# Kernel tuning notes

Hardware: AMD Instinct MI355X
Metric: run time of the kernel (lower is better)

Reference implementation:

```python
import jax, jax.numpy as jnp
import numpy as np
import math

DIM = 512
HEADS = 8
DHEAD = DIM // HEADS            # 64
NB_FEATURES = int(DHEAD * math.log(DHEAD))  # 266
B, N = 2, 2048
CHUNK = 128                     # chunk size for the causal scan
EPS = 1e-4


def gaussian_orthogonal_random_matrix(nb_rows, nb_cols, rng):
    # blocks of orthogonal rows (Q^T of QR of a gaussian), scaled by chi-distributed norms
    blocks = []
    n_full = nb_rows // nb_cols
    for _ in range(n_full):
        q, _ = np.linalg.qr(rng.standard_normal((nb_cols, nb_cols)))
        blocks.append(q.T)
    rem = nb_rows - n_full * nb_cols
    if rem > 0:
        q, _ = np.linalg.qr(rng.standard_normal((nb_cols, nb_cols)))
        blocks.append(q.T[:rem])
    mat = np.concatenate(blocks, axis=0)
    multiplier = np.linalg.norm(rng.standard_normal((nb_rows, nb_cols)), axis=1)
    return (multiplier[:, None] * mat).astype(np.float32)


def setup_inputs() -> dict:
    key = jax.random.key(0)
    k1, k2, k3 = jax.random.split(key, 3)
    rng = np.random.default_rng(0)
    x = jax.random.normal(k1, (B, N, DIM), dtype=jnp.float32)
    w_qkv = jax.random.normal(k2, (DIM, 3 * DIM), dtype=jnp.float32) / math.sqrt(DIM)
    w_out = jax.random.normal(k3, (DIM, DIM), dtype=jnp.float32) / math.sqrt(DIM)
    b_out = jnp.zeros((DIM,), dtype=jnp.float32)
    proj = jnp.asarray(gaussian_orthogonal_random_matrix(NB_FEATURES, DHEAD, rng))
    return {"x": x, "w_qkv": w_qkv, "w_out": w_out, "b_out": b_out, "proj": proj}


def softmax_kernel(data, proj, is_query):
    # data: [b,h,n,d], proj: [m,d]
    d = data.shape[-1]
    data_normalizer = d ** -0.25
    ratio = proj.shape[0] ** -0.5
    data_dash = jnp.einsum('bhnd,md->bhnm', data_normalizer * data, proj)
    diag_data = jnp.sum(data * data, axis=-1, keepdims=True) * 0.5 * (data_normalizer ** 2)
    if is_query:
        stab = jnp.max(data_dash, axis=-1, keepdims=True)
    else:
        stab = jnp.max(data_dash)
    return ratio * (jnp.exp(data_dash - diag_data - stab) + EPS)


def causal_linear_attention(q, k, v, chunk=CHUNK):
    # q,k: [b,h,n,m]; v: [b,h,n,d]
    # out_n = sum_m q_nm * (sum_{i<=n} k_im v_i) / (sum_{i<=n} k_im)   (per-feature normalization,
    # identical to causal_linear_attention_noncuda), computed in chunks for memory efficiency.
    b, h, n, m = q.shape
    d = v.shape[-1]
    nc = n // chunk
    qc = jnp.moveaxis(q.reshape(b, h, nc, chunk, m), 2, 0)  # [nc,b,h,C,m]
    kc = jnp.moveaxis(k.reshape(b, h, nc, chunk, m), 2, 0)
    vc = jnp.moveaxis(v.reshape(b, h, nc, chunk, d), 2, 0)

    def step(carry, inp):
        kv_state, ksum_state = carry            # [b,h,m,d], [b,h,m]
        qch, kch, vch = inp                     # [b,h,C,m], [b,h,C,m], [b,h,C,d]
        ksum = ksum_state[:, :, None, :] + jnp.cumsum(kch, axis=2)          # [b,h,C,m]
        ctx = kv_state[:, :, None, :, :] + jnp.cumsum(
            jnp.einsum('bhcm,bhcd->bhcmd', kch, vch), axis=2)               # [b,h,C,m,d]
        out = jnp.einsum('bhcm,bhcmd->bhcd', qch, ctx / ksum[..., None])
        return (ctx[:, :, -1], ksum[:, :, -1]), out

    init = (jnp.zeros((b, h, m, d), q.dtype), jnp.zeros((b, h, m), q.dtype))
    _, outs = jax.lax.scan(step, init, (qc, kc, vc))
    return jnp.moveaxis(outs, 0, 2).reshape(b, h, n, d)


def reference(x, w_qkv, w_out, b_out, proj):
    b, n, _ = x.shape
    qkv = x @ w_qkv                                   # [b,n,3*dim]
    q, k, v = jnp.split(qkv, 3, axis=-1)
    split = lambda t: t.reshape(b, n, HEADS, DHEAD).transpose(0, 2, 1, 3)  # b h n d
    q, k, v = split(q), split(k), split(v)
    qp = softmax_kernel(q, proj, is_query=True)       # [b,h,n,m]
    kp = softmax_kernel(k, proj, is_query=False)
    out = causal_linear_attention(qp, kp, v)          # [b,h,n,d]
    out = out.transpose(0, 2, 1, 3).reshape(b, n, DIM)
    return out @ w_out + b_out
```

## Files before the change

kernel.cpp:

```cpp
#include <hip/hip_runtime.h>
#include <math.h>

#define DIMX 512
#define NHEADS 8
#define DH 64
#define MF 266
#define MP 272
#define MPS 288
#define NB 2
#define NSEQ 2048
#define NROWS (NB*NSEQ)
#define NBH 16
#define CHK 64
#define NCH 32
#define EPSF 1e-4f
#define LDT 40
#define LDP 72

typedef __attribute__((ext_vector_type(8))) short short8;
typedef __attribute__((ext_vector_type(4))) float f32x4;
typedef unsigned short ushort_t;

__device__ __forceinline__ unsigned fkey(float f){
    unsigned u = __float_as_uint(f);
    return (f < 0.0f) ? ~u : (u | 0x80000000u);
}
__device__ __forceinline__ float fdec(unsigned k){
    unsigned u = (k & 0x80000000u) ? (k & 0x7fffffffu) : ~k;
    return __uint_as_float(u);
}
__device__ __forceinline__ float b2f(ushort_t u){
    return __uint_as_float(((unsigned)u) << 16);
}

__device__ __forceinline__ void bsplit(float a, ushort_t& h, ushort_t& l){
    unsigned u = __float_as_uint(a);
    unsigned r = (u + 0x7fffu + ((u >> 16) & 1u)) & 0xffff0000u;
    h = (ushort_t)(r >> 16);
    float res = a - __uint_as_float(r);
    unsigned v = __float_as_uint(res);
    unsigned r2 = v + 0x7fffu + ((v >> 16) & 1u);
    l = (ushort_t)(r2 >> 16);
}

__global__ __launch_bounds__(256) void split_kernel(
    const float* __restrict__ A, ushort_t* __restrict__ H, ushort_t* __restrict__ L, int total4)
{
    int i = blockIdx.x * 256 + threadIdx.x;
    if (i >= total4) return;
    float4 f = ((const float4*)A)[i];
    ushort_t h0,h1,h2,h3,l0,l1,l2,l3;
    bsplit(f.x,h0,l0); bsplit(f.y,h1,l1); bsplit(f.z,h2,l2); bsplit(f.w,h3,l3);
    ((ushort4*)H)[i] = make_ushort4(h0,h1,h2,h3);
    ((ushort4*)L)[i] = make_ushort4(l0,l1,l2,l3);
}

__global__ __launch_bounds__(256) void splitT_kernel(
    const float* __restrict__ W, ushort_t* __restrict__ Th, ushort_t* __restrict__ Tl,
    int K, int N)
{
    __shared__ ushort_t Sh[64][72], Sl[64][72];
    const int k0 = blockIdx.y * 64, n0 = blockIdx.x * 64;
    const int tid = threadIdx.x;
    {
        const int kk = tid >> 4, nq = (tid & 15) * 4;
        for (int p = 0; p < 4; p++) {
            int k = p*16 + kk;
            float4 f = *(const float4*)&W[(size_t)(k0 + k)*N + n0 + nq];
            ushort_t h, l;
            bsplit(f.x,h,l); Sh[nq+0][k]=h; Sl[nq+0][k]=l;
            bsplit(f.y,h,l); Sh[nq+1][k]=h; Sl[nq+1][k]=l;
            bsplit(f.z,h,l); Sh[nq+2][k]=h; Sl[nq+2][k]=l;
            bsplit(f.w,h,l); Sh[nq+3][k]=h; Sl[nq+3][k]=l;
        }
    }
    __syncthreads();
    {
        const int n = tid >> 2, ks = (tid & 3) * 16;
        for (int q = 0; q < 2; q++) {
            uint4 vh = *(const uint4*)&Sh[n][ks + q*8];
            uint4 vl = *(const uint4*)&Sl[n][ks + q*8];
            *(uint4*)&Th[(size_t)(n0 + n)*K + k0 + ks + q*8] = vh;
            *(uint4*)&Tl[(size_t)(n0 + n)*K + k0 + ks + q*8] = vl;
        }
    }
}

__global__ __launch_bounds__(256) void splitP_kernel(
    const float* __restrict__ proj, ushort_t* __restrict__ ph, ushort_t* __restrict__ pl,
    float nrm)
{
    int idx = blockIdx.x * 256 + threadIdx.x;
    if (idx >= MPS*64/4) return;
    int m = idx >> 4, kq = (idx & 15) * 4;
    ushort4 h4 = make_ushort4(0,0,0,0), l4 = make_ushort4(0,0,0,0);
    if (m < MF) {
        float4 f = *(const float4*)&proj[m*64 + kq];
        ushort_t hh[4], ll[4];
        bsplit(f.x*nrm,hh[0],ll[0]); bsplit(f.y*nrm,hh[1],ll[1]);
        bsplit(f.z*nrm,hh[2],ll[2]); bsplit(f.w*nrm,hh[3],ll[3]);
        h4 = make_ushort4(hh[0],hh[1],hh[2],hh[3]);
        l4 = make_ushort4(ll[0],ll[1],ll[2],ll[3]);
    }
    *(ushort4*)&ph[(size_t)m*64 + kq] = h4;
    *(ushort4*)&pl[(size_t)m*64 + kq] = l4;
}

__global__ __launch_bounds__(256) void gemm_bf16s(
    const ushort_t* __restrict__ Ah, const ushort_t* __restrict__ Al,
    const ushort_t* __restrict__ Bh, const ushort_t* __restrict__ Bl,
    const float* __restrict__ bias, float* __restrict__ C,
    int M, int N, int K)
{
    __shared__ ushort_t sAh[128*LDT], sAl[128*LDT], sBh[128*LDT], sBl[128*LDT];
    const int tid = threadIdx.x;
    const int m0 = blockIdx.y * 128, n0 = blockIdx.x * 128;
    const int lane = tid & 63, w = tid >> 6;
    const int wr = w >> 1, wc = w & 1;
    const int lr = lane & 15;
    const int lsu = (lane >> 4) * 8;
    const int r = tid >> 1, sg = (tid & 1) * 16;
    const size_t gA = (size_t)(m0 + r)*K + sg;
    const size_t gB = (size_t)(n0 + r)*K + sg;

    f32x4 acc[4][4];
    #pragma unroll
    for (int i=0;i<4;i++)
        #pragma unroll
        for (int j=0;j<4;j++) acc[i][j] = (f32x4){0.f,0.f,0.f,0.f};

    for (int k0 = 0; k0 < K; k0 += 32) {
        uint4 a0 = *(const uint4*)&Ah[gA + k0];
        uint4 a1 = *(const uint4*)&Ah[gA + k0 + 8];
        uint4 a2 = *(const uint4*)&Al[gA + k0];
        uint4 a3 = *(const uint4*)&Al[gA + k0 + 8];
        uint4 b0 = *(const uint4*)&Bh[gB + k0];
        uint4 b1 = *(const uint4*)&Bh[gB + k0 + 8];
        uint4 b2 = *(const uint4*)&Bl[gB + k0];
        uint4 b3 = *(const uint4*)&Bl[gB + k0 + 8];
        __syncthreads();
        *(uint4*)&sAh[r*LDT + sg]     = a0;
        *(uint4*)&sAh[r*LDT + sg + 8] = a1;
        *(uint4*)&sAl[r*LDT + sg]     = a2;
        *(uint4*)&sAl[r*LDT + sg + 8] = a3;
        *(uint4*)&sBh[r*LDT + sg]     = b0;
        *(uint4*)&sBh[r*LDT + sg + 8] = b1;
        *(uint4*)&sBl[r*LDT + sg]     = b2;
        *(uint4*)&sBl[r*LDT + sg + 8] = b3;
        __syncthreads();
        short8 afh[4], afl[4], bfh[4], bfl[4];
        #pragma unroll
        for (int f = 0; f < 4; f++) {
            int ra = (wr*64 + f*16 + lr)*LDT + lsu;
            int rb = (wc*64 + f*16 + lr)*LDT + lsu;
            afh[f] = *(const short8*)&sAh[ra];
            afl[f] = *(const short8*)&sAl[ra];
            bfh[f] = *(const short8*)&sBh[rb];
            bfl[f] = *(const short8*)&sBl[rb];
        }
        #pragma unroll
        for (int i = 0; i < 4; i++)
            #pragma unroll
            for (int j = 0; j < 4; j++) {
                acc[i][j] = __builtin_amdgcn_mfma_f32_16x16x32_bf16(afh[i], bfh[j], acc[i][j], 0, 0, 0);
                acc[i][j] = __builtin_amdgcn_mfma_f32_16x16x32_bf16(afh[i], bfl[j], acc[i][j], 0, 0, 0);
                acc[i][j] = __builtin_amdgcn_mfma_f32_16x16x32_bf16(afl[i], bfh[j], acc[i][j], 0, 0, 0);
            }
    }
    const int crow = (lane >> 4) * 4, ccol = lane & 15;
    #pragma unroll
    for (int i = 0; i < 4; i++) {
        #pragma unroll
        for (int j = 0; j < 4; j++) {
            int col = n0 + wc*64 + j*16 + ccol;
            float bb = bias ? bias[col] : 0.f;
            #pragma unroll
            for (int rr = 0; rr < 4; rr++) {
                int row = m0 + wr*64 + i*16 + crow + rr;
                C[(size_t)row*N + col] = acc[i][j][rr] + bb;
            }
        }
    }
}

template<bool IS_Q>
__global__ __launch_bounds__(256) void feat_mfma(
    const float* __restrict__ qkv,
    const ushort_t* __restrict__ pjh, const ushort_t* __restrict__ pjl,
    ushort_t* __restrict__ oh, ushort_t* __restrict__ ol,
    float* __restrict__ diag_out, unsigned* __restrict__ gmax,
    int coff, float ratio)
{
    __shared__ ushort_t sDh[64*LDP], sDl[64*LDP];
    __shared__ ushort_t sPh[32*LDP], sPl[32*LDP];
    __shared__ float dsqs[64];
    const int tid = threadIdx.x;
    const int bh = blockIdx.y, b = bh >> 3, h = bh & 7;
    const int n0 = blockIdx.x * 64;
    {
        const int r = tid >> 2, sgq = (tid & 3) * 16;
        const float* src = &qkv[(size_t)(b*NSEQ + n0 + r)*(3*DIMX) + coff + h*DH + sgq];
        float vals[16];
        float ss = 0.f;
        #pragma unroll
        for (int p = 0; p < 4; p++) {
            float4 f = *(const float4*)&src[p*4];
            vals[p*4+0]=f.x; vals[p*4+1]=f.y; vals[p*4+2]=f.z; vals[p*4+3]=f.w;
            ss = fmaf(f.x,f.x, fmaf(f.y,f.y, fmaf(f.z,f.z, fmaf(f.w,f.w, ss))));
        }
        ss += __shfl_xor(ss, 1, 64);
        ss += __shfl_xor(ss, 2, 64);
        if ((tid & 3) == 0) dsqs[r] = ss;
        #pragma unroll
        for (int p = 0; p < 16; p++) {
            ushort_t hh2, ll2;
            bsplit(vals[p], hh2, ll2);
            sDh[r*LDP + sgq + p] = hh2;
            sDl[r*LDP + sgq + p] = ll2;
        }
    }
    __syncthreads();
    const int lane = tid & 63, w = tid >> 6;
    const int fr = lane & 15, fk = (lane >> 4) * 8;
    short8 aDh[2], aDl[2];
    #pragma unroll
    for (int ks = 0; ks < 2; ks++) {
        int ra = (w*16 + fr)*LDP + ks*32 + fk;
        aDh[ks] = *(const short8*)&sDh[ra];
        aDl[ks] = *(const short8*)&sDl[ra];
    }
    f32x4 acc[18];
    #pragma unroll
    for (int t = 0; t < 18; t++) acc[t] = (f32x4){0.f,0.f,0.f,0.f};
    #pragma unroll
    for (int it = 0; it < 9; it++) {
        const int m0 = it*32;
        __syncthreads();
        {
            int r2 = tid >> 3, sg2 = (tid & 7) * 8;
            *(uint4*)&sPh[r2*LDP + sg2] = *(const uint4*)&pjh[(size_t)(m0 + r2)*64 + sg2];
            *(uint4*)&sPl[r2*LDP + sg2] = *(const uint4*)&pjl[(size_t)(m0 + r2)*64 + sg2];
        }
        __syncthreads();
        #pragma unroll
        for (int mt = 0; mt < 2; mt++) {
            short8 bh_[2], bl_[2];
            #pragma unroll
            for (int ks = 0; ks < 2; ks++) {
                int rb = (mt*16 + fr)*LDP + ks*32 + fk;
                bh_[ks] = *(const short8*)&sPh[rb];
                bl_[ks] = *(const short8*)&sPl[rb];
            }
            #pragma unroll
            for (int ks = 0; ks < 2; ks++) {
                acc[it*2+mt] = __builtin_amdgcn_mfma_f32_16x16x32_bf16(aDh[ks], bh_[ks], acc[it*2+mt], 0, 0, 0);
                acc[it*2+mt] = __builtin_amdgcn_mfma_f32_16x16x32_bf16(aDh[ks], bl_[ks], acc[it*2+mt], 0, 0, 0);
                acc[it*2+mt] = __builtin_amdgcn_mfma_f32_16x16x32_bf16(aDl[ks], bh_[ks], acc[it*2+mt], 0, 0, 0);
            }
        }
    }
    const size_t rbase = (size_t)bh*NSEQ + n0;
    const int crow = (lane >> 4) * 4, ccol = lane & 15;
    const int rw = w*16 + crow;
    float dg0[4];
    #pragma unroll
    for (int rr = 0; rr < 4; rr++) dg0[rr] = 0.0625f * dsqs[rw + rr];

    if (IS_Q) {
        #pragma unroll
        for (int rr = 0; rr < 4; rr++) {
            float mx = -1e30f;
            #pragma unroll
            for (int t = 0; t < 18; t++) {
                bool valid = (t < 16) || (t == 16 && ccol < (MF - 256));
                if (valid) mx = fmaxf(mx, acc[t][rr]);
            }
            mx = fmaxf(mx, __shfl_xor(mx, 1, 64));
            mx = fmaxf(mx, __shfl_xor(mx, 2, 64));
            mx = fmaxf(mx, __shfl_xor(mx, 4, 64));
            mx = fmaxf(mx, __shfl_xor(mx, 8, 64));
            float sub = dg0[rr] + mx;
            ushort_t* orh = &oh[(rbase + rw + rr)*MPS + ccol];
            ushort_t* orl = &ol[(rbase + rw + rr)*MPS + ccol];
            #pragma unroll
            for (int t = 0; t < 18; t++) {
                bool valid = (t < 16) || (t == 16 && ccol < (MF - 256));
                float v = valid ? ratio*(expf(acc[t][rr] - sub) + EPSF) : 0.f;
                ushort_t hh2, ll2; bsplit(v, hh2, ll2);
                orh[t*16] = hh2; orl[t*16] = ll2;
            }
        }
    } else {
        float wmax = -1e30f;
        #pragma unroll
        for (int rr = 0; rr < 4; rr++) {
            if (ccol == 0) diag_out[rbase + rw + rr] = dg0[rr];
            ushort_t* orh = &oh[(rbase + rw + rr)*MPS + ccol];
            ushort_t* orl = &ol[(rbase + rw + rr)*MPS + ccol];
            #pragma unroll
            for (int t = 0; t < 18; t++) {
                float v = acc[t][rr];
                bool valid = (t < 16) || (t == 16 && ccol < (MF - 256));
                if (valid) wmax = fmaxf(wmax, v);
                ushort_t hh2, ll2; bsplit(v, hh2, ll2);
                orh[t*16] = hh2; orl[t*16] = ll2;
            }
        }
        #pragma unroll
        for (int o = 1; o < 64; o <<= 1) wmax = fmaxf(wmax, __shfl_xor(wmax, o, 64));
        if (lane == 0) atomicMax(gmax, fkey(wmax));
    }
}

__global__ __launch_bounds__(256) void kexp_kernel(
    ushort_t* __restrict__ kph, ushort_t* __restrict__ kpl,
    const float* __restrict__ diagk, const unsigned* __restrict__ gmax, float ratio)
{
    unsigned gid = blockIdx.x * 256u + threadIdx.x;
    if (gid >= (unsigned)(NBH*NSEQ*(MPS/4))) return;
    unsigned row = gid / (MPS/4);
    int mq = (int)(gid % (MPS/4)) * 4;
    const float stab = fdec(*gmax);
    const float dg = diagk[row];
    size_t idx = (size_t)row*MPS + mq;
    ushort4 h4 = *(const ushort4*)&kph[idx];
    ushort4 l4 = *(const ushort4*)&kpl[idx];
    float dv[4] = {b2f(h4.x)+b2f(l4.x), b2f(h4.y)+b2f(l4.y),
                   b2f(h4.z)+b2f(l4.z), b2f(h4.w)+b2f(l4.w)};
    ushort_t hh[4], ll[4];
    #pragma unroll
    for (int j = 0; j < 4; j++) {
        float kv = (mq + j < MF) ? ratio * (expf(dv[j] - dg - stab) + EPSF) : 0.f;
        bsplit(kv, hh[j], ll[j]);
    }
    *(ushort4*)&kph[idx] = make_ushort4(hh[0],hh[1],hh[2],hh[3]);
    *(ushort4*)&kpl[idx] = make_ushort4(ll[0],ll[1],ll[2],ll[3]);
}

__global__ __launch_bounds__(320) void chunk_sums_kernel(
    const ushort_t* __restrict__ kph, const ushort_t* __restrict__ kpl,
    const float* __restrict__ qkv,
    float* __restrict__ ckvT, float* __restrict__ cksum)
{
    __shared__ float vs[CHK][DH];
    const int tid = threadIdx.x;
    const int c = blockIdx.x, bh = blockIdx.y, b = bh >> 3, h = bh & 7;
    for (int idx = tid; idx < CHK*16; idx += 320) {
        int i = idx >> 4, q = idx & 15;
        *(float4*)&vs[i][q*4] =
            *(const float4*)&qkv[(size_t)(b*NSEQ + c*CHK + i)*(3*DIMX) + 2*DIMX + h*DH + q*4];
    }
    __syncthreads();
    if (tid >= 272) return;
    const int mg = tid % 68, dg = tid / 68;
    float acc[4][16] = {};
    float ks[4] = {0.f,0.f,0.f,0.f};
    const size_t kbase = (size_t)(bh*NSEQ + c*CHK)*MPS + mg*4;
    for (int i = 0; i < CHK; i++) {
        ushort4 kh = *(const ushort4*)&kph[kbase + (size_t)i*MPS];
        ushort4 kl = *(const ushort4*)&kpl[kbase + (size_t)i*MPS];
        float kr[4] = {b2f(kh.x)+b2f(kl.x), b2f(kh.y)+b2f(kl.y),
                       b2f(kh.z)+b2f(kl.z), b2f(kh.w)+b2f(kl.w)};
        if (dg == 0) { ks[0]+=kr[0]; ks[1]+=kr[1]; ks[2]+=kr[2]; ks[3]+=kr[3]; }
        #pragma unroll
        for (int t = 0; t < 4; t++) {
            float4 vv = *(const float4*)&vs[i][dg*16 + t*4];
            float vr[4] = {vv.x,vv.y,vv.z,vv.w};
            #pragma unroll
            for (int mi=0;mi<4;mi++){
                acc[mi][t*4+0] = fmaf(kr[mi], vr[0], acc[mi][t*4+0]);
                acc[mi][t*4+1] = fmaf(kr[mi], vr[1], acc[mi][t*4+1]);
                acc[mi][t*4+2] = fmaf(kr[mi], vr[2], acc[mi][t*4+2]);
                acc[mi][t*4+3] = fmaf(kr[mi], vr[3], acc[mi][t*4+3]);
            }
        }
    }
    const size_t tbase = (size_t)(bh*NCH + c)*64;
    #pragma unroll
    for (int dd = 0; dd < 16; dd++) {
        int d = dg*16 + dd;
        *(float4*)&ckvT[(tbase + d)*MP + mg*4] =
            make_float4(acc[0][dd], acc[1][dd], acc[2][dd], acc[3][dd]);
    }
    if (dg == 0) {
        #pragma unroll
        for (int mi=0;mi<4;mi++)
            cksum[(size_t)(bh*NCH + c)*MP + mg*4 + mi] = ks[mi];
    }
}

__global__ __launch_bounds__(256) void prefix_ckvT_kernel(
    const float* __restrict__ ckvT, ushort_t* __restrict__ cth, ushort_t* __restrict__ ctl)
{
    const int bh = blockIdx.y;
    const int dm = blockIdx.x * 256 + threadIdx.x;
    if (dm >= 64*MPS) return;
    const int d = dm / MPS, m = dm % MPS;
    if (m < MP) {
        float run = 0.f;
        #pragma unroll
        for (int c = 0; c < NCH; c++) {
            size_t row = (size_t)(bh*NCH + c)*64 + d;
            ushort_t h, l;
            bsplit(run, h, l);
            cth[row*MPS + m] = h; ctl[row*MPS + m] = l;
            run += ckvT[row*MP + m];
        }
    } else {
        #pragma unroll
        for (int c = 0; c < NCH; c++) {
            size_t row = (size_t)(bh*NCH + c)*64 + d;
            cth[row*MPS + m] = 0; ctl[row*MPS + m] = 0;
        }
    }
}

__global__ __launch_bounds__(320) void prefix_ksum_kernel(float* __restrict__ cksum)
{
    const int bh = blockIdx.x;
    const int m = threadIdx.x;
    if (m >= MP) return;
    float run = 0.f;
    #pragma unroll
    for (int c = 0; c < NCH; c++) {
        size_t idx = (size_t)(bh*NCH + c)*MP + m;
        float v = cksum[idx];
        cksum[idx] = run;
        run += v;
    }
}

__global__ __launch_bounds__(320) void qprime_kernel(
    ushort_t* __restrict__ qph, ushort_t* __restrict__ qpl,
    const ushort_t* __restrict__ kph, const ushort_t* __restrict__ kpl,
    const float* __restrict__ cksum)
{
    const int c = blockIdx.x, bh = blockIdx.y;
    const int m = threadIdx.x;
    if (m >= MPS) return;
    size_t base = (size_t)(bh*NSEQ + c*CHK)*MPS + m;
    if (m < MF) {
        float run = cksum[(size_t)(bh*NCH + c)*MP + m];
        for (int i = 0; i < CHK; i++) {
            size_t idx = base + (size_t)i*MPS;
            run += b2f(kph[idx]) + b2f(kpl[idx]);
            float q = b2f(qph[idx]) + b2f(qpl[idx]);
            q /= run;
            ushort_t h, l;
            bsplit(q, h, l);
            qph[idx] = h; qpl[idx] = l;
        }
    } else {
        for (int i = 0; i < CHK; i++) {
            size_t idx = base + (size_t)i*MPS;
            qph[idx] = 0; qpl[idx] = 0;
        }
    }
}

__global__ __launch_bounds__(256) void attn_mfma(
    const ushort_t* __restrict__ qph, const ushort_t* __restrict__ qpl,
    const ushort_t* __restrict__ kph, const ushort_t* __restrict__ kpl,
    const ushort_t* __restrict__ cth, const ushort_t* __restrict__ ctl,
    const float* __restrict__ qkv,
    ushort_t* __restrict__ aout_h, ushort_t* __restrict__ aout_l)
{
    __shared__ ushort_t tQh[64*LDT], tQl[64*LDT];
    __shared__ ushort_t tKh[64*LDT], tKl[64*LDT];
    __shared__ ushort_t tSh[64*LDT], tSl[64*LDT];
    __shared__ ushort_t VTh[64*LDP], VTl[64*LDP];
    __shared__ ushort_t Ph[64*LDP],  Pl[64*LDP];
    const int tid = threadIdx.x;
    const int c = blockIdx.x, bh = blockIdx.y, b = bh >> 3, hh = bh & 7;
    const size_t rowg = (size_t)bh*NSEQ + c*CHK;
    const size_t rowx = (size_t)b*NSEQ + c*CHK;
    const size_t sbase = (size_t)(bh*NCH + c)*64;

    {
        const int j = tid >> 2, dq = (tid & 3) * 16;
        const float* vsrc = &qkv[(rowx + j)*(3*DIMX) + 2*DIMX + hh*DH + dq];
        #pragma unroll
        for (int p = 0; p < 4; p++) {
            float4 f = *(const float4*)&vsrc[p*4];
            float vr[4] = {f.x,f.y,f.z,f.w};
            #pragma unroll
            for (int wv = 0; wv < 4; wv++) {
                ushort_t h, l;
                bsplit(vr[wv], h, l);
                VTh[(dq + p*4 + wv)*LDP + j] = h;
                VTl[(dq + p*4 + wv)*LDP + j] = l;
            }
        }
    }

    const int lane = tid & 63, w = tid >> 6;
    const int wr = w >> 1, wc = w & 1;
    const int fr = lane & 15, fk = (lane >> 4) * 8;
    const int srow = tid >> 2, sseg = (tid & 3) * 8;
    f32x4 accP[2][2], accO[2][2];
    #pragma unroll
    for (int i=0;i<2;i++)
        #pragma unroll
        for (int j=0;j<2;j++){ accP[i][j]=(f32x4){0,0,0,0}; accO[i][j]=(f32x4){0,0,0,0}; }

    for (int m0 = 0; m0 < MPS; m0 += 32) {
        uint4 gq_h = *(const uint4*)&qph[(rowg + srow)*MPS + m0 + sseg];
        uint4 gq_l = *(const uint4*)&qpl[(rowg + srow)*MPS + m0 + sseg];
        uint4 gk_h = *(const uint4*)&kph[(rowg + srow)*MPS + m0 + sseg];
        uint4 gk_l = *(const uint4*)&kpl[(rowg + srow)*MPS + m0 + sseg];
        uint4 gs_h = *(const uint4*)&cth[(sbase + srow)*MPS + m0 + sseg];
        uint4 gs_l = *(const uint4*)&ctl[(sbase + srow)*MPS + m0 + sseg];
        __syncthreads();
        *(uint4*)&tQh[srow*LDT + sseg] = gq_h;
        *(uint4*)&tQl[srow*LDT + sseg] = gq_l;
        *(uint4*)&tKh[srow*LDT + sseg] = gk_h;
        *(uint4*)&tKl[srow*LDT + sseg] = gk_l;
        *(uint4*)&tSh[srow*LDT + sseg] = gs_h;
        *(uint4*)&tSl[srow*LDT + sseg] = gs_l;
        __syncthreads();
        short8 aQh[2], aQl[2], bKh[2], bKl[2], bSh[2], bSl[2];
        #pragma unroll
        for (int f = 0; f < 2; f++) {
            int ra = (wr*32 + f*16 + fr)*LDT + fk;
            int rb = (wc*32 + f*16 + fr)*LDT + fk;
            aQh[f] = *(const short8*)&tQh[ra];
            aQl[f] = *(const short8*)&tQl[ra];
            bKh[f] = *(const short8*)&tKh[rb];
            bKl[f] = *(const short8*)&tKl[rb];
            bSh[f] = *(const short8*)&tSh[rb];
            bSl[f] = *(const short8*)&tSl[rb];
        }
        #pragma unroll
        for (int i = 0; i < 2; i++)
            #pragma unroll
            for (int j = 0; j < 2; j++) {
                accP[i][j] = __builtin_amdgcn_mfma_f32_16x16x32_bf16(aQh[i], bKh[j], accP[i][j], 0, 0, 0);
                accP[i][j] = __builtin_amdgcn_mfma_f32_16x16x32_bf16(aQh[i], bKl[j], accP[i][j], 0, 0, 0);
                accP[i][j] = __builtin_amdgcn_mfma_f32_16x16x32_bf16(aQl[i], bKh[j], accP[i][j], 0, 0, 0);
                accO[i][j] = __builtin_amdgcn_mfma_f32_16x16x32_bf16(aQh[i], bSh[j], accO[i][j], 0, 0, 0);
                accO[i][j] = __builtin_amdgcn_mfma_f32_16x16x32_bf16(aQh[i], bSl[j], accO[i][j], 0, 0, 0);
                accO[i][j] = __builtin_amdgcn_mfma_f32_16x16x32_bf16(aQl[i], bSh[j], accO[i][j], 0, 0, 0);
            }
    }

    __syncthreads();
    {
        const int crow = (lane >> 4) * 4, ccol = lane & 15;
        #pragma unroll
        for (int i = 0; i < 2; i++)
            #pragma unroll
            for (int j = 0; j < 2; j++) {
                int colg = wc*32 + j*16 + ccol;
                #pragma unroll
                for (int rr = 0; rr < 4; rr++) {
                    int rowg2 = wr*32 + i*16 + crow + rr;
                    float v = (colg <= rowg2) ? accP[i][j][rr] : 0.f;
                    ushort_t h, l;
                    bsplit(v, h, l);
                    Ph[rowg2*LDP + colg] = h;
                    Pl[rowg2*LDP + colg] = l;
                }
            }
    }
    __syncthreads();

    #pragma unroll
    for (int js = 0; js < 2; js++) {
        short8 aPh[2], aPl[2], bVh[2], bVl[2];
        #pragma unroll
        for (int f = 0; f < 2; f++) {
            int ra = (wr*32 + f*16 + fr)*LDP + js*32 + fk;
            int rb = (wc*32 + f*16 + fr)*LDP + js*32 + fk;
            aPh[f] = *(const short8*)&Ph[ra];
            aPl[f] = *(const short8*)&Pl[ra];
            bVh[f] = *(const short8*)&VTh[rb];
            bVl[f] = *(const short8*)&VTl[rb];
        }
        #pragma unroll
        for (int i = 0; i < 2; i++)
            #pragma unroll
            for (int j = 0; j < 2; j++) {
                accO[i][j] = __builtin_amdgcn_mfma_f32_16x16x32_bf16(aPh[i], bVh[j], accO[i][j], 0, 0, 0);
                accO[i][j] = __builtin_amdgcn_mfma_f32_16x16x32_bf16(aPh[i], bVl[j], accO[i][j], 0, 0, 0);
                accO[i][j] = __builtin_amdgcn_mfma_f32_16x16x32_bf16(aPl[i], bVh[j], accO[i][j], 0, 0, 0);
            }
    }

    {
        const int crow = (lane >> 4) * 4, ccol = lane & 15;
        #pragma unroll
        for (int i = 0; i < 2; i++)
            #pragma unroll
            for (int j = 0; j < 2; j++) {
                int d = wc*32 + j*16 + ccol;
                #pragma unroll
                for (int rr = 0; rr < 4; rr++) {
                    int row = wr*32 + i*16 + crow + rr;
                    size_t o = (rowx + row)*DIMX + hh*DH + d;
                    ushort_t h, l;
                    bsplit(accO[i][j][rr], h, l);
                    aout_h[o] = h; aout_l[o] = l;
                }
            }
    }
}

extern "C" void kernel_launch(void* const* d_in, const int* in_sizes, int n_in,
                              void* d_out, int out_size, void* d_ws, size_t ws_size,
                              hipStream_t stream)
{
    (void)in_sizes; (void)n_in; (void)out_size; (void)ws_size;
    const float* x     = (const float*)d_in[0];
    const float* w_qkv = (const float*)d_in[1];
    const float* w_out = (const float*)d_in[2];
    const float* b_out = (const float*)d_in[3];
    const float* proj  = (const float*)d_in[4];
    float* out = (float*)d_out;

    char* ws = (char*)d_ws;
    size_t off = 0;
    auto alloc = [&](size_t bytes) -> char* {
        char* p = ws + off;
        off += (bytes + 255) & ~(size_t)255;
        return p;
    };
    float* qkv       = (float*)alloc((size_t)NROWS*3*DIMX*sizeof(float));
    float* ckvT      = (float*)alloc((size_t)NBH*NCH*64*MP*sizeof(float));
    ushort_t* qph    = (ushort_t*)alloc((size_t)NBH*NSEQ*MPS*sizeof(ushort_t));
    ushort_t* qpl    = (ushort_t*)alloc((size_t)NBH*NSEQ*MPS*sizeof(ushort_t));
    ushort_t* kph    = (ushort_t*)alloc((size_t)NBH*NSEQ*MPS*sizeof(ushort_t));
    ushort_t* kpl    = (ushort_t*)alloc((size_t)NBH*NSEQ*MPS*sizeof(ushort_t));
    ushort_t* cth    = (ushort_t*)alloc((size_t)NBH*NCH*64*MPS*sizeof(ushort_t));
    ushort_t* ctl    = (ushort_t*)alloc((size_t)NBH*NCH*64*MPS*sizeof(ushort_t));
    float* cksum     = (float*)alloc((size_t)NBH*NCH*MP*sizeof(float));
    float* diagk     = (float*)alloc((size_t)NBH*NSEQ*sizeof(float));
    unsigned* gmax   = (unsigned*)alloc(256);
    ushort_t* xs_h   = (ushort_t*)alloc((size_t)NROWS*DIMX*sizeof(ushort_t));
    ushort_t* xs_l   = (ushort_t*)alloc((size_t)NROWS*DIMX*sizeof(ushort_t));
    ushort_t* wqt_h  = (ushort_t*)alloc((size_t)(3*DIMX)*DIMX*sizeof(ushort_t));
    ushort_t* wqt_l  = (ushort_t*)alloc((size_t)(3*DIMX)*DIMX*sizeof(ushort_t));
    ushort_t* wot_h  = (ushort_t*)alloc((size_t)DIMX*DIMX*sizeof(ushort_t));
    ushort_t* wot_l  = (ushort_t*)alloc((size_t)DIMX*DIMX*sizeof(ushort_t));
    ushort_t* pjh    = (ushort_t*)alloc((size_t)MPS*64*sizeof(ushort_t));
    ushort_t* pjl    = (ushort_t*)alloc((size_t)MPS*64*sizeof(ushort_t));
    ushort_t* aout_h = xs_h;
    ushort_t* aout_l = xs_l;

    const float nrm   = (float)pow(64.0, -0.25);
    const float ratio = (float)(1.0 / sqrt(266.0));

    hipMemsetAsync(gmax, 0, sizeof(unsigned), stream);
    split_kernel<<<dim3((NROWS*DIMX/4 + 255)/256), 256, 0, stream>>>(x, xs_h, xs_l, NROWS*DIMX/4);
    splitT_kernel<<<dim3(3*DIMX/64, DIMX/64), 256, 0, stream>>>(w_qkv, wqt_h, wqt_l, DIMX, 3*DIMX);
    splitT_kernel<<<dim3(DIMX/64, DIMX/64), 256, 0, stream>>>(w_out, wot_h, wot_l, DIMX, DIMX);
    splitP_kernel<<<dim3((MPS*64/4 + 255)/256), 256, 0, stream>>>(proj, pjh, pjl, nrm);
    gemm_bf16s<<<dim3(3*DIMX/128, NROWS/128), 256, 0, stream>>>(
        xs_h, xs_l, wqt_h, wqt_l, nullptr, qkv, NROWS, 3*DIMX, DIMX);
    feat_mfma<true ><<<dim3(32, 16), 256, 0, stream>>>(
        qkv, pjh, pjl, qph, qpl, nullptr, nullptr, 0, ratio);
    feat_mfma<false><<<dim3(32, 16), 256, 0, stream>>>(
        qkv, pjh, pjl, kph, kpl, diagk, gmax, DIMX, ratio);
    kexp_kernel<<<dim3((NBH*NSEQ*(MPS/4) + 255)/256), 256, 0, stream>>>(
        kph, kpl, diagk, gmax, ratio);
    chunk_sums_kernel<<<dim3(NCH, NBH), 320, 0, stream>>>(kph, kpl, qkv, ckvT, cksum);
    prefix_ckvT_kernel<<<dim3((64*MPS + 255)/256, NBH), 256, 0, stream>>>(ckvT, cth, ctl);
    prefix_ksum_kernel<<<dim3(NBH), 320, 0, stream>>>(cksum);
    qprime_kernel<<<dim3(NCH, NBH), 320, 0, stream>>>(qph, qpl, kph, kpl, cksum);
    attn_mfma<<<dim3(NCH, NBH), 256, 0, stream>>>(
        qph, qpl, kph, kpl, cth, ctl, qkv, aout_h, aout_l);
    gemm_bf16s<<<dim3(DIMX/128, NROWS/128), 256, 0, stream>>>(
        aout_h, aout_l, wot_h, wot_l, b_out, out, NROWS, DIMX, DIMX);
}
```

Before: 248.6 us.

## Stage feature and attention outputs through LDS for coalesced stores; double-buffer projection tiles

The feature kernel now double-buffers the projection tiles in one shared buffer. Each next tile's load is issued after the current tile's MFMAs, which drops one of the two barriers per iteration. The bf16 hi/lo feature outputs were previously written as scattered 2-byte global stores. They are now staged in LDS and written as 16-byte row-contiguous stores, with the lo halves packed into registers so the same LDS buffer can be reused. The attention kernel's output also goes through LDS for vectorized stores. This adds extra barriers, LDS traffic and register pressure from the 36-entry pack array.

```diff
diff --git a/kernel.cpp b/kernel.cpp
--- a/kernel.cpp
+++ b/kernel.cpp
@@ -16,6 +16,7 @@
 #define EPSF 1e-4f
 #define LDT 40
 #define LDP 72
+#define LDO 296
 
 typedef __attribute__((ext_vector_type(8))) short short8;
 typedef __attribute__((ext_vector_type(4))) float f32x4;
@@ -191,9 +192,12 @@
     float* __restrict__ diag_out, unsigned* __restrict__ gmax,
     int coff, float ratio)
 {
-    __shared__ ushort_t sDh[64*LDP], sDl[64*LDP];
-    __shared__ ushort_t sPh[32*LDP], sPl[32*LDP];
+    __shared__ ushort_t smem[64*LDO];
     __shared__ float dsqs[64];
+    ushort_t* sDh = smem;
+    ushort_t* sDl = smem + 64*LDP;
+    ushort_t* sP  = smem + 2*64*LDP;
+    ushort_t* outb = smem;
     const int tid = threadIdx.x;
     const int bh = blockIdx.y, b = bh >> 3, h = bh & 7;
     const int n0 = blockIdx.x * 64;
@@ -219,6 +223,11 @@
             sDl[r*LDP + sgq + p] = ll2;
         }
     }
+    {
+        const int r2 = tid >> 3, sg2 = (tid & 7) * 8;
+        *(uint4*)&sP[r2*LDP + sg2]        = *(const uint4*)&pjh[(size_t)r2*64 + sg2];
+        *(uint4*)&sP[2304 + r2*LDP + sg2] = *(const uint4*)&pjl[(size_t)r2*64 + sg2];
+    }
     __syncthreads();
     const int lane = tid & 63, w = tid >> 6;
     const int fr = lane & 15, fk = (lane >> 4) * 8;
@@ -234,22 +243,16 @@
     for (int t = 0; t < 18; t++) acc[t] = (f32x4){0.f,0.f,0.f,0.f};
     #pragma unroll
     for (int it = 0; it < 9; it++) {
-        const int m0 = it*32;
-        __syncthreads();
-        {
-            int r2 = tid >> 3, sg2 = (tid & 7) * 8;
-            *(uint4*)&sPh[r2*LDP + sg2] = *(const uint4*)&pjh[(size_t)(m0 + r2)*64 + sg2];
-            *(uint4*)&sPl[r2*LDP + sg2] = *(const uint4*)&pjl[(size_t)(m0 + r2)*64 + sg2];
-        }
-        __syncthreads();
+        const ushort_t* bufh = sP + (it & 1) * 4608;
+        const ushort_t* bufl = bufh + 2304;
         #pragma unroll
         for (int mt = 0; mt < 2; mt++) {
             short8 bh_[2], bl_[2];
             #pragma unroll
             for (int ks = 0; ks < 2; ks++) {
                 int rb = (mt*16 + fr)*LDP + ks*32 + fk;
-                bh_[ks] = *(const short8*)&sPh[rb];
-                bl_[ks] = *(const short8*)&sPl[rb];
+                bh_[ks] = *(const short8*)&bufh[rb];
+                bl_[ks] = *(const short8*)&bufl[rb];
             }
             #pragma unroll
             for (int ks = 0; ks < 2; ks++) {
@@ -258,6 +261,13 @@
                 acc[it*2+mt] = __builtin_amdgcn_mfma_f32_16x16x32_bf16(aDl[ks], bh_[ks], acc[it*2+mt], 0, 0, 0);
             }
         }
+        if (it < 8) {
+            const int r2 = tid >> 3, sg2 = (tid & 7) * 8;
+            ushort_t* nb = sP + ((it+1) & 1) * 4608;
+            *(uint4*)&nb[r2*LDP + sg2]        = *(const uint4*)&pjh[(size_t)((it+1)*32 + r2)*64 + sg2];
+            *(uint4*)&nb[2304 + r2*LDP + sg2] = *(const uint4*)&pjl[(size_t)((it+1)*32 + r2)*64 + sg2];
+        }
+        __syncthreads();
     }
     const size_t rbase = (size_t)bh*NSEQ + n0;
     const int crow = (lane >> 4) * 4, ccol = lane & 15;
@@ -265,6 +275,7 @@
     float dg0[4];
     #pragma unroll
     for (int rr = 0; rr < 4; rr++) dg0[rr] = 0.0625f * dsqs[rw + rr];
+    unsigned lpack[36];
 
     if (IS_Q) {
         #pragma unroll
@@ -280,14 +291,14 @@
             mx = fmaxf(mx, __shfl_xor(mx, 4, 64));
             mx = fmaxf(mx, __shfl_xor(mx, 8, 64));
             float sub = dg0[rr] + mx;
-            ushort_t* orh = &oh[(rbase + rw + rr)*MPS + ccol];
-            ushort_t* orl = &ol[(rbase + rw + rr)*MPS + ccol];
             #pragma unroll
             for (int t = 0; t < 18; t++) {
                 bool valid = (t < 16) || (t == 16 && ccol < (MF - 256));
                 float v = valid ? ratio*(expf(acc[t][rr] - sub) + EPSF) : 0.f;
                 ushort_t hh2, ll2; bsplit(v, hh2, ll2);
-                orh[t*16] = hh2; orl[t*16] = ll2;
+                outb[(rw + rr)*LDO + t*16 + ccol] = hh2;
+                if ((t & 1) == 0) lpack[rr*9 + t/2] = ll2;
+                else              lpack[rr*9 + t/2] |= ((unsigned)ll2) << 16;
             }
         }
     } else {
@@ -295,20 +306,41 @@
         #pragma unroll
         for (int rr = 0; rr < 4; rr++) {
             if (ccol == 0) diag_out[rbase + rw + rr] = dg0[rr];
-            ushort_t* orh = &oh[(rbase + rw + rr)*MPS + ccol];
-            ushort_t* orl = &ol[(rbase + rw + rr)*MPS + ccol];
             #pragma unroll
             for (int t = 0; t < 18; t++) {
                 float v = acc[t][rr];
                 bool valid = (t < 16) || (t == 16 && ccol < (MF - 256));
                 if (valid) wmax = fmaxf(wmax, v);
                 ushort_t hh2, ll2; bsplit(v, hh2, ll2);
-                orh[t*16] = hh2; orl[t*16] = ll2;
+                outb[(rw + rr)*LDO + t*16 + ccol] = hh2;
+                if ((t & 1) == 0) lpack[rr*9 + t/2] = ll2;
+                else              lpack[rr*9 + t/2] |= ((unsigned)ll2) << 16;
             }
         }
         #pragma unroll
         for (int o = 1; o < 64; o <<= 1) wmax = fmaxf(wmax, __shfl_xor(wmax, o, 64));
         if (lane == 0) atomicMax(gmax, fkey(wmax));
+    }
+    __syncthreads();
+    #pragma unroll
+    for (int p = 0; p < 9; p++) {
+        int u = tid + p*256;
+        int row = u / 36, c8 = u % 36;
+        *(uint4*)&oh[(rbase + row)*MPS + c8*8] = *(const uint4*)&outb[row*LDO + c8*8];
+    }
+    __syncthreads();
+    #pragma unroll
+    for (int rr = 0; rr < 4; rr++)
+        #pragma unroll
+        for (int t = 0; t < 18; t++)
+            outb[(rw + rr)*LDO + t*16 + ccol] =
+                (ushort_t)((lpack[rr*9 + t/2] >> (16*(t & 1))) & 0xffffu);
+    __syncthreads();
+    #pragma unroll
+    for (int p = 0; p < 9; p++) {
+        int u = tid + p*256;
+        int row = u / 36, c8 = u % 36;
+        *(uint4*)&ol[(rbase + row)*MPS + c8*8] = *(const uint4*)&outb[row*LDO + c8*8];
     }
 }
 
@@ -586,6 +618,7 @@
             }
     }
 
+    __syncthreads();
     {
         const int crow = (lane >> 4) * 4, ccol = lane & 15;
         #pragma unroll
@@ -596,12 +629,21 @@
                 #pragma unroll
                 for (int rr = 0; rr < 4; rr++) {
                     int row = wr*32 + i*16 + crow + rr;
-                    size_t o = (rowx + row)*DIMX + hh*DH + d;
                     ushort_t h, l;
                     bsplit(accO[i][j][rr], h, l);
-                    aout_h[o] = h; aout_l[o] = l;
+                    Ph[row*LDP + d] = h;
+                    Pl[row*LDP + d] = l;
                 }
             }
+    }
+    __syncthreads();
+    #pragma unroll
+    for (int p = 0; p < 2; p++) {
+        int u = tid + p*256;
+        int row = u >> 3, c8 = u & 7;
+        size_t o = (rowx + row)*DIMX + hh*DH + c8*8;
+        *(uint4*)&aout_h[o] = *(const uint4*)&Ph[row*LDP + c8*8];
+        *(uint4*)&aout_l[o] = *(const uint4*)&Pl[row*LDP + c8*8];
     }
 }
 
```

Result: no change. 250.0 us (+0.5%).

## Merge Q/K feature kernels and stage outputs through LDS for coalesced stores

Applied to the files above, without the earlier changes.

Merges the query and key feature-map kernels into one launch that picks Q or K from blockIdx.z. Data fragments are now loaded straight into registers and projection fragments are read directly from global memory, replacing the staged LDS tiles and their barrier loops. Both the feature kernel and the attention epilogue now write results into shared memory first and then issue 16-byte coalesced global stores instead of scattered 2-byte stores. The cost is extra LDS (about 75 KB in the feature kernel, which may lower occupancy) and uncoalesced global reads of the projection matrix.

```diff
diff --git a/kernel.cpp b/kernel.cpp
--- a/kernel.cpp
+++ b/kernel.cpp
@@ -16,6 +16,7 @@
 #define EPSF 1e-4f
 #define LDT 40
 #define LDP 72
+#define LDO 296
 
 typedef __attribute__((ext_vector_type(8))) short short8;
 typedef __attribute__((ext_vector_type(4))) float f32x4;
@@ -183,90 +184,76 @@
     }
 }
 
-template<bool IS_Q>
-__global__ __launch_bounds__(256) void feat_mfma(
+__global__ __launch_bounds__(256) void feat_mfma2(
     const float* __restrict__ qkv,
     const ushort_t* __restrict__ pjh, const ushort_t* __restrict__ pjl,
-    ushort_t* __restrict__ oh, ushort_t* __restrict__ ol,
-    float* __restrict__ diag_out, unsigned* __restrict__ gmax,
-    int coff, float ratio)
-{
-    __shared__ ushort_t sDh[64*LDP], sDl[64*LDP];
-    __shared__ ushort_t sPh[32*LDP], sPl[32*LDP];
+    ushort_t* __restrict__ qph, ushort_t* __restrict__ qpl,
+    ushort_t* __restrict__ kph, ushort_t* __restrict__ kpl,
+    float* __restrict__ diag_out, unsigned* __restrict__ gmax, float ratio)
+{
+    __shared__ ushort_t outH[64*LDO];
+    __shared__ ushort_t outL[64*LDO];
     __shared__ float dsqs[64];
     const int tid = threadIdx.x;
+    const bool isq = (blockIdx.z == 0);
+    const int coff = isq ? 0 : DIMX;
+    ushort_t* __restrict__ oh = isq ? qph : kph;
+    ushort_t* __restrict__ ol = isq ? qpl : kpl;
     const int bh = blockIdx.y, b = bh >> 3, h = bh & 7;
     const int n0 = blockIdx.x * 64;
+    const int lane = tid & 63, w = tid >> 6;
+    const int fr = lane & 15, fj = lane >> 4;
+
+    short8 aDh[2], aDl[2];
     {
-        const int r = tid >> 2, sgq = (tid & 3) * 16;
-        const float* src = &qkv[(size_t)(b*NSEQ + n0 + r)*(3*DIMX) + coff + h*DH + sgq];
-        float vals[16];
+        const int row = w*16 + fr;
+        const float* src = &qkv[(size_t)(b*NSEQ + n0 + row)*(3*DIMX) + coff + h*DH];
+        float4 u0 = *(const float4*)&src[fj*8];
+        float4 u1 = *(const float4*)&src[fj*8 + 4];
+        float4 u2 = *(const float4*)&src[32 + fj*8];
+        float4 u3 = *(const float4*)&src[32 + fj*8 + 4];
+        float v0[8] = {u0.x,u0.y,u0.z,u0.w,u1.x,u1.y,u1.z,u1.w};
+        float v1[8] = {u2.x,u2.y,u2.z,u2.w,u3.x,u3.y,u3.z,u3.w};
         float ss = 0.f;
         #pragma unroll
-        for (int p = 0; p < 4; p++) {
-            float4 f = *(const float4*)&src[p*4];
-            vals[p*4+0]=f.x; vals[p*4+1]=f.y; vals[p*4+2]=f.z; vals[p*4+3]=f.w;
-            ss = fmaf(f.x,f.x, fmaf(f.y,f.y, fmaf(f.z,f.z, fmaf(f.w,f.w, ss))));
-        }
-        ss += __shfl_xor(ss, 1, 64);
-        ss += __shfl_xor(ss, 2, 64);
-        if ((tid & 3) == 0) dsqs[r] = ss;
-        #pragma unroll
-        for (int p = 0; p < 16; p++) {
+        for (int p = 0; p < 8; p++) ss = fmaf(v0[p],v0[p], fmaf(v1[p],v1[p], ss));
+        ss += __shfl_xor(ss, 16, 64);
+        ss += __shfl_xor(ss, 32, 64);
+        if (fj == 0) dsqs[row] = ss;
+        #pragma unroll
+        for (int p = 0; p < 8; p++) {
             ushort_t hh2, ll2;
-            bsplit(vals[p], hh2, ll2);
-            sDh[r*LDP + sgq + p] = hh2;
-            sDl[r*LDP + sgq + p] = ll2;
-        }
-    }
-    __syncthreads();
-    const int lane = tid & 63, w = tid >> 6;
-    const int fr = lane & 15, fk = (lane >> 4) * 8;
-    short8 aDh[2], aDl[2];
-    #pragma unroll
-    for (int ks = 0; ks < 2; ks++) {
-        int ra = (w*16 + fr)*LDP + ks*32 + fk;
-        aDh[ks] = *(const short8*)&sDh[ra];
-        aDl[ks] = *(const short8*)&sDl[ra];
+            bsplit(v0[p], hh2, ll2); aDh[0][p] = (short)hh2; aDl[0][p] = (short)ll2;
+            bsplit(v1[p], hh2, ll2); aDh[1][p] = (short)hh2; aDl[1][p] = (short)ll2;
+        }
     }
     f32x4 acc[18];
     #pragma unroll
     for (int t = 0; t < 18; t++) acc[t] = (f32x4){0.f,0.f,0.f,0.f};
     #pragma unroll
-    for (int it = 0; it < 9; it++) {
-        const int m0 = it*32;
-        __syncthreads();
-        {
-            int r2 = tid >> 3, sg2 = (tid & 7) * 8;
-            *(uint4*)&sPh[r2*LDP + sg2] = *(const uint4*)&pjh[(size_t)(m0 + r2)*64 + sg2];
-            *(uint4*)&sPl[r2*LDP + sg2] = *(const uint4*)&pjl[(size_t)(m0 + r2)*64 + sg2];
-        }
-        __syncthreads();
-        #pragma unroll
-        for (int mt = 0; mt < 2; mt++) {
-            short8 bh_[2], bl_[2];
-            #pragma unroll
-            for (int ks = 0; ks < 2; ks++) {
-                int rb = (mt*16 + fr)*LDP + ks*32 + fk;
-                bh_[ks] = *(const short8*)&sPh[rb];
-                bl_[ks] = *(const short8*)&sPl[rb];
-            }
-            #pragma unroll
-            for (int ks = 0; ks < 2; ks++) {
-                acc[it*2+mt] = __builtin_amdgcn_mfma_f32_16x16x32_bf16(aDh[ks], bh_[ks], acc[it*2+mt], 0, 0, 0);
-                acc[it*2+mt] = __builtin_amdgcn_mfma_f32_16x16x32_bf16(aDh[ks], bl_[ks], acc[it*2+mt], 0, 0, 0);
-                acc[it*2+mt] = __builtin_amdgcn_mfma_f32_16x16x32_bf16(aDl[ks], bh_[ks], acc[it*2+mt], 0, 0, 0);
-            }
-        }
-    }
+    for (int mt = 0; mt < 18; mt++) {
+        const size_t rb = (size_t)(mt*16 + fr)*64 + fj*8;
+        short8 bh_[2], bl_[2];
+        bh_[0] = *(const short8*)&pjh[rb];
+        bh_[1] = *(const short8*)&pjh[rb + 32];
+        bl_[0] = *(const short8*)&pjl[rb];
+        bl_[1] = *(const short8*)&pjl[rb + 32];
+        #pragma unroll
+        for (int ks = 0; ks < 2; ks++) {
+            acc[mt] = __builtin_amdgcn_mfma_f32_16x16x32_bf16(aDh[ks], bh_[ks], acc[mt], 0, 0, 0);
+            acc[mt] = __builtin_amdgcn_mfma_f32_16x16x32_bf16(aDh[ks], bl_[ks], acc[mt], 0, 0, 0);
+            acc[mt] = __builtin_amdgcn_mfma_f32_16x16x32_bf16(aDl[ks], bh_[ks], acc[mt], 0, 0, 0);
+        }
+    }
+    __syncthreads();
     const size_t rbase = (size_t)bh*NSEQ + n0;
-    const int crow = (lane >> 4) * 4, ccol = lane & 15;
-    const int rw = w*16 + crow;
+    const int ccol = fr;
+    const int rw = w*16 + fj*4;
     float dg0[4];
     #pragma unroll
     for (int rr = 0; rr < 4; rr++) dg0[rr] = 0.0625f * dsqs[rw + rr];
 
-    if (IS_Q) {
+    if (isq) {
         #pragma unroll
         for (int rr = 0; rr < 4; rr++) {
             float mx = -1e30f;
@@ -280,14 +267,13 @@
             mx = fmaxf(mx, __shfl_xor(mx, 4, 64));
             mx = fmaxf(mx, __shfl_xor(mx, 8, 64));
             float sub = dg0[rr] + mx;
-            ushort_t* orh = &oh[(rbase + rw + rr)*MPS + ccol];
-            ushort_t* orl = &ol[(rbase + rw + rr)*MPS + ccol];
             #pragma unroll
             for (int t = 0; t < 18; t++) {
                 bool valid = (t < 16) || (t == 16 && ccol < (MF - 256));
                 float v = valid ? ratio*(expf(acc[t][rr] - sub) + EPSF) : 0.f;
                 ushort_t hh2, ll2; bsplit(v, hh2, ll2);
-                orh[t*16] = hh2; orl[t*16] = ll2;
+                outH[(rw + rr)*LDO + t*16 + ccol] = hh2;
+                outL[(rw + rr)*LDO + t*16 + ccol] = ll2;
             }
         }
     } else {
@@ -295,20 +281,27 @@
         #pragma unroll
         for (int rr = 0; rr < 4; rr++) {
             if (ccol == 0) diag_out[rbase + rw + rr] = dg0[rr];
-            ushort_t* orh = &oh[(rbase + rw + rr)*MPS + ccol];
-            ushort_t* orl = &ol[(rbase + rw + rr)*MPS + ccol];
             #pragma unroll
             for (int t = 0; t < 18; t++) {
                 float v = acc[t][rr];
                 bool valid = (t < 16) || (t == 16 && ccol < (MF - 256));
                 if (valid) wmax = fmaxf(wmax, v);
                 ushort_t hh2, ll2; bsplit(v, hh2, ll2);
-                orh[t*16] = hh2; orl[t*16] = ll2;
+                outH[(rw + rr)*LDO + t*16 + ccol] = hh2;
+                outL[(rw + rr)*LDO + t*16 + ccol] = ll2;
             }
         }
         #pragma unroll
         for (int o = 1; o < 64; o <<= 1) wmax = fmaxf(wmax, __shfl_xor(wmax, o, 64));
         if (lane == 0) atomicMax(gmax, fkey(wmax));
+    }
+    __syncthreads();
+    #pragma unroll
+    for (int p = 0; p < 9; p++) {
+        int u = tid + p*256;
+        int row = u / 36, c8 = u % 36;
+        *(uint4*)&oh[(rbase + row)*MPS + c8*8] = *(const uint4*)&outH[row*LDO + c8*8];
+        *(uint4*)&ol[(rbase + row)*MPS + c8*8] = *(const uint4*)&outL[row*LDO + c8*8];
     }
 }
 
@@ -586,6 +579,7 @@
             }
     }
 
+    __syncthreads();
     {
         const int crow = (lane >> 4) * 4, ccol = lane & 15;
         #pragma unroll
@@ -596,12 +590,21 @@
                 #pragma unroll
                 for (int rr = 0; rr < 4; rr++) {
                     int row = wr*32 + i*16 + crow + rr;
-                    size_t o = (rowx + row)*DIMX + hh*DH + d;
                     ushort_t h, l;
                     bsplit(accO[i][j][rr], h, l);
-                    aout_h[o] = h; aout_l[o] = l;
+                    Ph[row*LDP + d] = h;
+                    Pl[row*LDP + d] = l;
                 }
             }
+    }
+    __syncthreads();
+    #pragma unroll
+    for (int p = 0; p < 2; p++) {
+        int u = tid + p*256;
+        int row = u >> 3, c8 = u & 7;
+        size_t o = (rowx + row)*DIMX + hh*DH + c8*8;
+        *(uint4*)&aout_h[o] = *(const uint4*)&Ph[row*LDP + c8*8];
+        *(uint4*)&aout_l[o] = *(const uint4*)&Pl[row*LDP + c8*8];
     }
 }
 
@@ -656,10 +659,8 @@
     splitP_kernel<<<dim3((MPS*64/4 + 255)/256), 256, 0, stream>>>(proj, pjh, pjl, nrm);
     gemm_bf16s<<<dim3(3*DIMX/128, NROWS/128), 256, 0, stream>>>(
         xs_h, xs_l, wqt_h, wqt_l, nullptr, qkv, NROWS, 3*DIMX, DIMX);
-    feat_mfma<true ><<<dim3(32, 16), 256, 0, stream>>>(
-        qkv, pjh, pjl, qph, qpl, nullptr, nullptr, 0, ratio);
-    feat_mfma<false><<<dim3(32, 16), 256, 0, stream>>>(
-        qkv, pjh, pjl, kph, kpl, diagk, gmax, DIMX, ratio);
+    feat_mfma2<<<dim3(32, 16, 2), 256, 0, stream>>>(
+        qkv, pjh, pjl, qph, qpl, kph, kpl, diagk, gmax, ratio);
     kexp_kernel<<<dim3((NBH*NSEQ*(MPS/4) + 255)/256), 256, 0, stream>>>(
         kph, kpl, diagk, gmax, ratio);
     chunk_sums_kernel<<<dim3(NCH, NBH), 320, 0, stream>>>(kph, kpl, qkv, ckvT, cksum);
```

Measured after the change: 260.1 us. 1.05x slower.
